# Kernel tuning notes

Hardware: AMD Instinct MI355X
Metric: run time of the kernel (lower is better)

Reference implementation:

```python
import jax, jax.numpy as jnp
import numpy as np

DIM = 32      # state dim (enc_shape[0])
LDIM = 256    # latent dim (enc_shape[-1])
N_AUX = LDIM // 2
AUX_H = 128   # aux hidden
ENC_H = 256   # encoder hidden
T = 64        # n_shifts
N = 1024      # batch
DT = 0.01


def setup_inputs() -> dict:
    key = jax.random.key(0)
    ks = jax.random.split(key, 13)
    def w(k, shape, fan):
        return jax.random.normal(k, shape, jnp.float32) / np.sqrt(fan).astype(np.float32)
    return {
        "xs": jax.random.normal(ks[0], (N, T, DIM), jnp.float32),
        # encoder MLP: dim -> 256 -> 256 -> ldim (last layer has no bias)
        "enc_W1": w(ks[1], (DIM, ENC_H), DIM), "enc_b1": w(ks[2], (ENC_H,), ENC_H),
        "enc_W2": w(ks[3], (ENC_H, ENC_H), ENC_H), "enc_b2": w(ks[4], (ENC_H,), ENC_H),
        "enc_W3": w(ks[5], (ENC_H, LDIM), ENC_H),
        # n_aux independent aux MLPs: dim -> 128 -> 128 -> 2 (last no bias), stacked
        "aux_W1": w(ks[6], (N_AUX, DIM, AUX_H), DIM), "aux_b1": w(ks[7], (N_AUX, AUX_H), AUX_H),
        "aux_W2": w(ks[8], (N_AUX, AUX_H, AUX_H), AUX_H), "aux_b2": w(ks[9], (N_AUX, AUX_H), AUX_H),
        "aux_W3": w(ks[10], (N_AUX, AUX_H, 2), AUX_H),
        # C: Linear(ldim, dim, bias=False); stored as [ldim, dim] so x_next = y @ C_W
        "C_W": w(ks[11], (LDIM, DIM), LDIM),
    }


def reference(xs, enc_W1, enc_b1, enc_W2, enc_b2, enc_W3,
              aux_W1, aux_b1, aux_W2, aux_b2, aux_W3, C_W):
    x0 = xs[:, 0, :]                                    # [N, dim]
    # all n_aux tiny MLPs batched via einsum (instead of python loop)
    h = jax.nn.relu(jnp.einsum('nd,kdh->nkh', x0, aux_W1) + aux_b1)
    h = jax.nn.relu(jnp.einsum('nkh,khg->nkg', h, aux_W2) + aux_b2)
    aux = jnp.einsum('nkh,kho->nko', h, aux_W3)          # [N, n_aux, 2] -> (mu, omega)
    scale = jnp.exp(aux[..., 0] * DT)
    cos = jnp.cos(aux[..., 1] * DT) * scale              # [N, n_aux]
    sin = jnp.sin(aux[..., 1] * DT) * scale

    # encoder over all n_shifts timesteps
    e = jax.nn.relu(xs @ enc_W1 + enc_b1)
    e = jax.nn.relu(e @ enc_W2 + enc_b2)
    e = e @ enc_W3                                       # [N, T, ldim]
    y = jnp.concatenate([xs, e], axis=-1)                # [N, T, dim+ldim]

    # Koopman recurrence. The original builds a block-diagonal [ldim, ldim]
    # matrix of 2x2 rotation-scaling blocks (block k acts on latent pair
    # (2k, 2k+1)) and applies it as a row-vector bmm: out = y_row @ K with
    # K_block = [[cos, sin], [-sin, cos]]. We apply the blocks directly.
    y0 = e[:, 0, :].reshape(N, N_AUX, 2)
    def step(carry, _):
        y1, y2 = carry[..., 0], carry[..., 1]
        yn = jnp.stack([y1 * cos - y2 * sin, y1 * sin + y2 * cos], axis=-1)
        return yn, yn
    _, ys = jax.lax.scan(step, y0, None, length=T - 1)   # [T-1, N, n_aux, 2]
    ys = jnp.moveaxis(ys, 0, 1).reshape(N, T - 1, LDIM)  # [N, T-1, ldim]

    y_lat = jnp.concatenate([e[:, :1, :], ys], axis=1)          # [N, T, ldim]
    x_pred = jnp.concatenate([xs[:, :1, :], ys @ C_W], axis=1)  # [N, T, dim]
    y_pred = jnp.concatenate([x_pred, y_lat], axis=-1)          # [N, T, dim+ldim]
    return y, y_pred
```

## Files before the change

kernel.cpp:

```cpp
#include <hip/hip_runtime.h>
#include <math.h>

#define N_SEQ 1024
#define T_SEQ 64
#define DIMX  32
#define LDIM  256
#define NAUX  128
#define AUXH  128
#define ENCH  256
#define OUTC  288
#define DT    0.01f

typedef short bf16x8 __attribute__((ext_vector_type(8)));
typedef float f32x4  __attribute__((ext_vector_type(4)));
typedef unsigned short ush;

__device__ __forceinline__ ush f2bf(float f) {
    unsigned u = __builtin_bit_cast(unsigned, f);
    unsigned r = u + 0x7fffu + ((u >> 16) & 1u);
    return (ush)(r >> 16);
}
__device__ __forceinline__ float bf2f(ush h) {
    unsigned u = ((unsigned)h) << 16;
    return __builtin_bit_cast(float, u);
}
__device__ __forceinline__ f32x4 mfma16(bf16x8 a, bf16x8 b, f32x4 c) {
    return __builtin_amdgcn_mfma_f32_16x16x32_bf16(a, b, c, 0, 0, 0);
}

#define CV_ENC   139264
#define PREP_CONV_BLOCKS 576
#define PREP_TR_BLOCKS   2560
#define PREP_ENC0_BLOCKS 256
__global__ __launch_bounds__(256) void prep_kernel(
    const float* __restrict__ eW1, const float* __restrict__ eb1,
    const float* __restrict__ eW2, const float* __restrict__ eb2,
    const float* __restrict__ eW3, const float* __restrict__ C_W,
    const float* __restrict__ aW1, const float* __restrict__ aW2,
    const float* __restrict__ xs,
    ush* __restrict__ encw, float* __restrict__ cwt,
    ush* __restrict__ a1h, ush* __restrict__ a1l,
    ush* __restrict__ a2h, ush* __restrict__ a2l,
    float* __restrict__ y)
{
    __shared__ float psm[1152];
    const int b   = blockIdx.x;
    const int tid = threadIdx.x;

    if (b < PREP_CONV_BLOCKS) {
        const int idx = b * 256 + tid;
        if (idx < 8192) {
            int c = idx >> 5, k = idx & 31;
            encw[idx] = f2bf(eW1[k * ENCH + c]);
        } else if (idx < 8192 + 65536) {
            int t = idx - 8192; int c = t >> 8, k = t & 255;
            encw[idx] = f2bf(eW2[k * ENCH + c]);
        } else if (idx < CV_ENC) {
            int t = idx - (8192 + 65536); int c = t >> 8, k = t & 255;
            encw[idx] = f2bf(eW3[k * LDIM + c]);
        } else if (idx < CV_ENC + 8192) {
            int t = idx - CV_ENC; int d = t >> 8, l = t & 255;
            cwt[t] = C_W[l * DIMX + d];
        }
        return;
    }

    if (b < PREP_CONV_BLOCKS + PREP_TR_BLOCKS) {
        float (*tile)[33] = (float(*)[33])psm;
        const int bb0 = b - PREP_CONV_BLOCKS;
        const float* src; ush *dh, *dl; int R, j0, r0;
        if (bb0 < 512) {
            int k = bb0 >> 2; j0 = (bb0 & 3) * 32; r0 = 0; R = 32;
            src = aW1 + (size_t)k * 4096;
            dh = a1h + (size_t)k * 4096; dl = a1l + (size_t)k * 4096;
        } else {
            int bb = bb0 - 512;
            int k = bb >> 4; j0 = ((bb >> 2) & 3) * 32; r0 = (bb & 3) * 32; R = 128;
            src = aW2 + (size_t)k * 16384;
            dh = a2h + (size_t)k * 16384; dl = a2l + (size_t)k * 16384;
        }
        for (int i = tid; i < 1024; i += 256) {
            int rr = i >> 5, jj = i & 31;
            tile[rr][jj] = src[(r0 + rr) * 128 + j0 + jj];
        }
        __syncthreads();
        for (int i = tid; i < 1024; i += 256) {
            int jj = i >> 5, rr = i & 31;
            float w = tile[rr][jj];
            ush hi = f2bf(w);
            int off = (j0 + jj) * R + r0 + rr;
            dh[off] = hi;
            dl[off] = f2bf(w - bf2f(hi));
        }
        return;
    }

    {
        float* Xs  = psm;
        float* Hsf = psm + 128;
        const int c  = tid;
        const int n0 = (b - PREP_CONV_BLOCKS - PREP_TR_BLOCKS) * 4;

        if (tid < 32) {
            int r = tid >> 3, q = tid & 7;
            *(float4*)&Xs[r * 32 + q * 4] =
                *(const float4*)&xs[(size_t)(n0 + r) * (T_SEQ * DIMX) + q * 4];
        }
        __syncthreads();

        float acc[4];
        {
            float w[32];
            #pragma unroll
            for (int d = 0; d < 32; ++d) w[d] = eW1[d * ENCH + c];
            const float bb = eb1[c];
            #pragma unroll
            for (int r = 0; r < 4; ++r) {
                float a = bb;
                #pragma unroll
                for (int d4 = 0; d4 < 8; ++d4) {
                    float4 xv = *(const float4*)&Xs[r * 32 + d4 * 4];
                    a += xv.x * w[d4*4] + xv.y * w[d4*4+1] + xv.z * w[d4*4+2] + xv.w * w[d4*4+3];
                }
                acc[r] = a;
            }
            #pragma unroll
            for (int r = 0; r < 4; ++r) Hsf[r * 256 + c] = fmaxf(acc[r], 0.f);
        }
        __syncthreads();
        {
            const float bb = eb2[c];
            #pragma unroll
            for (int r = 0; r < 4; ++r) acc[r] = bb;
            for (int hc = 0; hc < 8; ++hc) {
                float w[32];
                #pragma unroll
                for (int i = 0; i < 32; ++i) w[i] = eW2[(hc * 32 + i) * ENCH + c];
                #pragma unroll
                for (int r = 0; r < 4; ++r) {
                    float a = acc[r];
                    #pragma unroll
                    for (int h4 = 0; h4 < 8; ++h4) {
                        float4 hv = *(const float4*)&Hsf[r * 256 + hc * 32 + h4 * 4];
                        a += hv.x * w[h4*4] + hv.y * w[h4*4+1] + hv.z * w[h4*4+2] + hv.w * w[h4*4+3];
                    }
                    acc[r] = a;
                }
            }
            __syncthreads();
            #pragma unroll
            for (int r = 0; r < 4; ++r) Hsf[r * 256 + c] = fmaxf(acc[r], 0.f);
        }
        __syncthreads();
        {
            #pragma unroll
            for (int r = 0; r < 4; ++r) acc[r] = 0.f;
            for (int hc = 0; hc < 8; ++hc) {
                float w[32];
                #pragma unroll
                for (int i = 0; i < 32; ++i) w[i] = eW3[(hc * 32 + i) * LDIM + c];
                #pragma unroll
                for (int r = 0; r < 4; ++r) {
                    float a = acc[r];
                    #pragma unroll
                    for (int h4 = 0; h4 < 8; ++h4) {
                        float4 hv = *(const float4*)&Hsf[r * 256 + hc * 32 + h4 * 4];
                        a += hv.x * w[h4*4] + hv.y * w[h4*4+1] + hv.z * w[h4*4+2] + hv.w * w[h4*4+3];
                    }
                    acc[r] = a;
                }
            }
        }
        #pragma unroll
        for (int r = 0; r < 4; ++r)
            y[((size_t)(n0 + r) * T_SEQ) * OUTC + DIMX + c] = acc[r];
    }
}

__global__ __launch_bounds__(256) void main_kernel(
    const float* __restrict__ xs,
    const ush* __restrict__ W1h, const ush* __restrict__ W1l,
    const float* __restrict__ ab1,
    const ush* __restrict__ W2h, const ush* __restrict__ W2l,
    const float* __restrict__ ab2,
    const float* __restrict__ aW3,
    float* __restrict__ a_ws, float* __restrict__ th_ws,
    const ush* __restrict__ W1T, const float* __restrict__ eb1,
    const ush* __restrict__ W2T, const float* __restrict__ eb2,
    const ush* __restrict__ W3T,
    float* __restrict__ y)
{
    __shared__ __align__(16) char smem[46080];
    const int tid = threadIdx.x;
    const int wv  = tid >> 6;
    const int ln  = tid & 63;
    const int lr  = ln & 15;
    const int g   = ln >> 4;

    if (blockIdx.x < 2048) {
        ush (*x0h)[40]  = (ush(*)[40]) (smem);
        ush (*x0l)[40]  = (ush(*)[40]) (smem + 5120);
        ush (*h1h)[136] = (ush(*)[136])(smem + 10240);
        ush (*h1l)[136] = (ush(*)[136])(smem + 27648);
        float* p3       = (float*)     (smem + 45056);

        const int k   = blockIdx.x >> 4;
        const int n0  = (blockIdx.x & 15) << 6;
        const int cb  = wv * 32;

        for (int i = tid; i < 512; i += 256) {
            int r = i >> 3, qd = i & 7;
            float4 v = *(const float4*)&xs[(size_t)(n0 + r) * (T_SEQ * DIMX) + qd * 4];
            short4 hs, ls;
            float vv[4] = {v.x, v.y, v.z, v.w};
            short* hp = (short*)&hs; short* lp = (short*)&ls;
            #pragma unroll
            for (int u = 0; u < 4; ++u) {
                ush hi = f2bf(vv[u]);
                hp[u] = (short)hi;
                lp[u] = (short)f2bf(vv[u] - bf2f(hi));
            }
            *(short4*)&x0h[r][qd * 4] = hs;
            *(short4*)&x0l[r][qd * 4] = ls;
        }
        __syncthreads();

        {
            const ush* W1hk = W1h + (size_t)k * 4096;
            const ush* W1lk = W1l + (size_t)k * 4096;
            bf16x8 bh[2], bl[2];
            #pragma unroll
            for (int ct = 0; ct < 2; ++ct) {
                int off = (cb + ct * 16 + lr) * 32 + g * 8;
                bh[ct] = *(const bf16x8*)&W1hk[off];
                bl[ct] = *(const bf16x8*)&W1lk[off];
            }
            f32x4 acc[4][2];
            #pragma unroll
            for (int rt = 0; rt < 4; ++rt) {
                bf16x8 ah = *(const bf16x8*)&x0h[rt * 16 + lr][g * 8];
                bf16x8 al = *(const bf16x8*)&x0l[rt * 16 + lr][g * 8];
                #pragma unroll
                for (int ct = 0; ct < 2; ++ct) {
                    f32x4 z = {0.f, 0.f, 0.f, 0.f};
                    z = mfma16(ah, bl[ct], z);
                    z = mfma16(al, bh[ct], z);
                    acc[rt][ct] = mfma16(ah, bh[ct], z);
                }
            }
            #pragma unroll
            for (int ct = 0; ct < 2; ++ct) {
                const int col = cb + ct * 16 + lr;
                const float bb = ab1[k * 128 + col];
                #pragma unroll
                for (int rt = 0; rt < 4; ++rt)
                    #pragma unroll
                    for (int i = 0; i < 4; ++i) {
                        float h = fmaxf(acc[rt][ct][i] + bb, 0.f);
                        ush hi = f2bf(h);
                        int row = rt * 16 + g * 4 + i;
                        h1h[row][col] = hi;
                        h1l[row][col] = f2bf(h - bf2f(hi));
                    }
            }
        }
        __syncthreads();

        {
            const ush* W2hk = W2h + (size_t)k * 16384;
            const ush* W2lk = W2l + (size_t)k * 16384;
            f32x4 acc[4][2];
            #pragma unroll
            for (int rt = 0; rt < 4; ++rt)
                #pragma unroll
                for (int ct = 0; ct < 2; ++ct) acc[rt][ct] = (f32x4){0.f,0.f,0.f,0.f};

            #pragma unroll
            for (int kk = 0; kk < 4; ++kk) {
                bf16x8 bh[2], bl[2], ah[4], al[4];
                #pragma unroll
                for (int ct = 0; ct < 2; ++ct) {
                    int off = (cb + ct * 16 + lr) * 128 + kk * 32 + g * 8;
                    bh[ct] = *(const bf16x8*)&W2hk[off];
                    bl[ct] = *(const bf16x8*)&W2lk[off];
                }
                #pragma unroll
                for (int rt = 0; rt < 4; ++rt) {
                    ah[rt] = *(const bf16x8*)&h1h[rt * 16 + lr][kk * 32 + g * 8];
                    al[rt] = *(const bf16x8*)&h1l[rt * 16 + lr][kk * 32 + g * 8];
                }
                #pragma unroll
                for (int rt = 0; rt < 4; ++rt)
                    #pragma unroll
                    for (int ct = 0; ct < 2; ++ct) {
                        f32x4 z = acc[rt][ct];
                        z = mfma16(ah[rt], bl[ct], z);
                        z = mfma16(al[rt], bh[ct], z);
                        acc[rt][ct] = mfma16(ah[rt], bh[ct], z);
                    }
            }
            __syncthreads();
            #pragma unroll
            for (int ct = 0; ct < 2; ++ct) {
                const int col = cb + ct * 16 + lr;
                const float bb = ab2[k * 128 + col];
                #pragma unroll
                for (int rt = 0; rt < 4; ++rt)
                    #pragma unroll
                    for (int i = 0; i < 4; ++i) {
                        float h = fmaxf(acc[rt][ct][i] + bb, 0.f);
                        ush hi = f2bf(h);
                        int row = rt * 16 + g * 4 + i;
                        h1h[row][col] = hi;
                        h1l[row][col] = f2bf(h - bf2f(hi));
                    }
            }
        }
        __syncthreads();

        {
            const int hh = tid >> 7, r = tid & 127, n = r >> 1, o = r & 1;
            const float* W3k = aW3 + (size_t)k * (AUXH * 2);
            float s = 0.f;
            #pragma unroll
            for (int h8 = hh * 64; h8 < hh * 64 + 64; h8 += 8) {
                bf16x8 vh = *(const bf16x8*)&h1h[n][h8];
                bf16x8 vl = *(const bf16x8*)&h1l[n][h8];
                #pragma unroll
                for (int u = 0; u < 8; ++u) {
                    float hv = bf2f((ush)vh[u]) + bf2f((ush)vl[u]);
                    s += hv * W3k[(h8 + u) * 2 + o];
                }
            }
            p3[tid] = s;
        }
        __syncthreads();
        if (tid < 128) {
            const int n = tid >> 1, o = tid & 1;
            float v = (p3[tid] + p3[tid + 128]) * DT;
            float* dst = o ? th_ws : a_ws;
            dst[(size_t)(n0 + n) * NAUX + k] = v;
        }
        return;
    }

    {
        float* Xf = (float*)smem;
        ush*   Hs = (ush*)(smem + 9216);

        const int cb  = wv * 64;
        const size_t row0 = (size_t)(blockIdx.x - 2048) * 64;

        {
            const float4* src = (const float4*)(xs + row0 * DIMX);
            for (int i = tid; i < 512; i += 256) {
                int r = i >> 3, q = i & 7;
                *(float4*)&Xf[r * 36 + q * 4] = src[i];
            }
        }
        __syncthreads();

        {
            f32x4 acc[4][4];
            bf16x8 bfr[4], afr[4];
            #pragma unroll
            for (int ct = 0; ct < 4; ++ct)
                bfr[ct] = *(const bf16x8*)&W1T[(cb + ct * 16 + lr) * 32 + g * 8];
            #pragma unroll
            for (int rt = 0; rt < 4; ++rt) {
                const float* xp = &Xf[(rt * 16 + lr) * 36 + g * 8];
                float4 u = *(const float4*)xp;
                float4 v = *(const float4*)(xp + 4);
                bf16x8 t;
                t[0]=(short)f2bf(u.x); t[1]=(short)f2bf(u.y); t[2]=(short)f2bf(u.z); t[3]=(short)f2bf(u.w);
                t[4]=(short)f2bf(v.x); t[5]=(short)f2bf(v.y); t[6]=(short)f2bf(v.z); t[7]=(short)f2bf(v.w);
                afr[rt] = t;
            }
            #pragma unroll
            for (int rt = 0; rt < 4; ++rt)
                #pragma unroll
                for (int ct = 0; ct < 4; ++ct) {
                    f32x4 z = {0.f, 0.f, 0.f, 0.f};
                    acc[rt][ct] = mfma16(afr[rt], bfr[ct], z);
                }
            #pragma unroll
            for (int ct = 0; ct < 4; ++ct) {
                const float bb = eb1[cb + ct * 16 + lr];
                #pragma unroll
                for (int rt = 0; rt < 4; ++rt)
                    #pragma unroll
                    for (int i = 0; i < 4; ++i) {
                        float h = fmaxf(acc[rt][ct][i] + bb, 0.f);
                        Hs[(rt * 16 + g * 4 + i) * 264 + cb + ct * 16 + lr] = f2bf(h);
                    }
            }
        }
        __syncthreads();

        int wrow[4], hoff[4];
        #pragma unroll
        for (int ct = 0; ct < 4; ++ct) wrow[ct] = (cb + ct * 16 + lr) * 256 + g * 8;
        #pragma unroll
        for (int rt = 0; rt < 4; ++rt) hoff[rt] = (rt * 16 + lr) * 264 + g * 8;

        {
            f32x4 acc[4][4];
            #pragma unroll
            for (int rt = 0; rt < 4; ++rt)
                #pragma unroll
                for (int ct = 0; ct < 4; ++ct) acc[rt][ct] = (f32x4){0.f,0.f,0.f,0.f};
            #pragma unroll 2
            for (int kk = 0; kk < 8; ++kk) {
                bf16x8 bfr[4], afr[4];
                #pragma unroll
                for (int ct = 0; ct < 4; ++ct)
                    bfr[ct] = *(const bf16x8*)&W2T[wrow[ct] + kk * 32];
                #pragma unroll
                for (int rt = 0; rt < 4; ++rt)
                    afr[rt] = *(const bf16x8*)&Hs[hoff[rt] + kk * 32];
                #pragma unroll
                for (int rt = 0; rt < 4; ++rt)
                    #pragma unroll
                    for (int ct = 0; ct < 4; ++ct)
                        acc[rt][ct] = mfma16(afr[rt], bfr[ct], acc[rt][ct]);
            }
            __syncthreads();
            #pragma unroll
            for (int ct = 0; ct < 4; ++ct) {
                const float bb = eb2[cb + ct * 16 + lr];
                #pragma unroll
                for (int rt = 0; rt < 4; ++rt)
                    #pragma unroll
                    for (int i = 0; i < 4; ++i) {
                        float h = fmaxf(acc[rt][ct][i] + bb, 0.f);
                        Hs[(rt * 16 + g * 4 + i) * 264 + cb + ct * 16 + lr] = f2bf(h);
                    }
            }
        }
        __syncthreads();

        {
            f32x4 acc[4][4];
            #pragma unroll
            for (int rt = 0; rt < 4; ++rt)
                #pragma unroll
                for (int ct = 0; ct < 4; ++ct) acc[rt][ct] = (f32x4){0.f,0.f,0.f,0.f};
            #pragma unroll 2
            for (int kk = 0; kk < 8; ++kk) {
                bf16x8 bfr[4], afr[4];
                #pragma unroll
                for (int ct = 0; ct < 4; ++ct)
                    bfr[ct] = *(const bf16x8*)&W3T[wrow[ct] + kk * 32];
                #pragma unroll
                for (int rt = 0; rt < 4; ++rt)
                    afr[rt] = *(const bf16x8*)&Hs[hoff[rt] + kk * 32];
                #pragma unroll
                for (int rt = 0; rt < 4; ++rt)
                    #pragma unroll
                    for (int ct = 0; ct < 4; ++ct)
                        acc[rt][ct] = mfma16(afr[rt], bfr[ct], acc[rt][ct]);
            }
            __syncthreads();

            float* HsF = (float*)Hs;
            const int r  = tid >> 3;
            const int ce = tid & 7;

            #pragma unroll
            for (int p = 0; p < 2; ++p) {
                #pragma unroll
                for (int rt = 2 * p; rt < 2 * p + 2; ++rt)
                    #pragma unroll
                    for (int ct = 0; ct < 4; ++ct)
                        #pragma unroll
                        for (int i = 0; i < 4; ++i)
                            HsF[((rt - 2 * p) * 16 + g * 4 + i) * 264 + cb + ct * 16 + lr]
                                = acc[rt][ct][i];
                __syncthreads();
                const int rloc = p * 32 + r;
                float* dstrow = &y[(row0 + rloc) * OUTC];
                #pragma unroll
                for (int j = 0; j < 9; ++j) {
                    int f4 = j * 8 + ce;
                    float4 v;
                    if (f4 < 8) v = *(const float4*)&Xf[rloc * 36 + f4 * 4];
                    else        v = *(const float4*)&HsF[r * 264 + (f4 - 8) * 4];
                    if (!(rloc == 0 && f4 >= 8))
                        *(float4*)&dstrow[f4 * 4] = v;
                }
                __syncthreads();
            }
        }
    }
}

__global__ __launch_bounds__(256) void scan3_kernel(
    const float* __restrict__ xs,
    const float* __restrict__ a_ws, const float* __restrict__ th_ws,
    const float* __restrict__ cwt,
    const float* __restrict__ y,
    float* __restrict__ yp)
{
    __shared__ float ys_lds[16][256];

    const int n = blockIdx.x >> 2;
    const int q = blockIdx.x & 3;
    const int e = threadIdx.x;
    const int k = e >> 1;

    const float* yrow0 = y + (size_t)n * T_SEQ * OUTC + DIMX;
    float2 y0 = *(const float2*)&yrow0[e & ~1];
    const float a  = a_ws [n * NAUX + k];
    const float th = th_ws[n * NAUX + k];

    const float m = expf(a);
    float ss, cc; sincosf(th, &ss, &cc);
    const float zr = m * cc, zi = m * ss;

    float pr = zr, pi = zi;
    #pragma unroll
    for (int s2 = 0; s2 < 4; ++s2) {
        float nr = pr * pr - pi * pi;
        pi = 2.f * pr * pi; pr = nr;
    }
    float wr = 1.f, wi = 0.f;
    for (int j = 0; j < q; ++j) {
        float nr = wr * pr - wi * pi;
        wi = wr * pi + wi * pr; wr = nr;
    }

    const bool imag = e & 1;
    float* ypn = yp + (size_t)n * T_SEQ * OUTC;

    #pragma unroll 4
    for (int tl = 0; tl < 16; ++tl) {
        const int t = q * 16 + tl;
        float val = imag ? (y0.x * wi + y0.y * wr)
                         : (y0.x * wr - y0.y * wi);
        ypn[(size_t)t * OUTC + DIMX + e] = val;
        ys_lds[tl][(e + ((tl >> 1) & 7) * 4) & 255] = val;
        float nwr = wr * zr - wi * zi;
        wi = wr * zi + wi * zr;
        wr = nwr;
    }
    __syncthreads();

    const int d   = e >> 3;
    const int tg  = e & 7;
    const int tl0 = tg * 2, tl1 = tl0 + 1;
    const float* cwd = cwt + d * 256;
    const int rot = tg * 4;

    float s0 = 0.f, s1 = 0.f;
    #pragma unroll 8
    for (int l = 0; l < 256; l += 4) {
        const int c0 = (l + rot) & 255;
        float4 wv = *(const float4*)&cwd[l];
        float4 ya = *(const float4*)&ys_lds[tl0][c0];
        float4 yb = *(const float4*)&ys_lds[tl1][c0];
        s0 += ya.x * wv.x + ya.y * wv.y + ya.z * wv.z + ya.w * wv.w;
        s1 += yb.x * wv.x + yb.y * wv.y + yb.z * wv.z + yb.w * wv.w;
    }
    const int t0 = q * 16 + tl0;
    const int t1 = q * 16 + tl1;
    float o0 = (t0 == 0) ? xs[(size_t)n * T_SEQ * DIMX + d] : s0;
    ypn[(size_t)t0 * OUTC + d] = o0;
    ypn[(size_t)t1 * OUTC + d] = s1;
}

extern "C" void kernel_launch(void* const* d_in, const int* in_sizes, int n_in,
                              void* d_out, int out_size, void* d_ws, size_t ws_size,
                              hipStream_t stream)
{
    const float* xs   = (const float*)d_in[0];
    const float* eW1  = (const float*)d_in[1];
    const float* eb1  = (const float*)d_in[2];
    const float* eW2  = (const float*)d_in[3];
    const float* eb2  = (const float*)d_in[4];
    const float* eW3  = (const float*)d_in[5];
    const float* aW1  = (const float*)d_in[6];
    const float* ab1  = (const float*)d_in[7];
    const float* aW2  = (const float*)d_in[8];
    const float* ab2  = (const float*)d_in[9];
    const float* aW3  = (const float*)d_in[10];
    const float* C_W  = (const float*)d_in[11];

    float* y  = (float*)d_out;
    float* yp = y + (size_t)N_SEQ * T_SEQ * OUTC;

    float* a_ws  = (float*)d_ws;
    float* th_ws = a_ws + (size_t)N_SEQ * NAUX;
    ush* encw = (ush*)(th_ws + (size_t)N_SEQ * NAUX);
    ush* W1T = encw;
    ush* W2T = encw + 8192;
    ush* W3T = encw + 8192 + 65536;
    ush* a1h = encw + CV_ENC;
    ush* a1l = a1h + 524288;
    ush* a2h = a1l + 524288;
    ush* a2l = a2h + 2097152;
    float* cwt = (float*)(a2l + 2097152);

    prep_kernel<<<PREP_CONV_BLOCKS + PREP_TR_BLOCKS + PREP_ENC0_BLOCKS, 256, 0, stream>>>(
        eW1, eb1, eW2, eb2, eW3, C_W, aW1, aW2, xs,
        encw, cwt, a1h, a1l, a2h, a2l, y);
    main_kernel<<<3072, 256, 0, stream>>>(
        xs, a1h, a1l, ab1, a2h, a2l, ab2, aW3, a_ws, th_ws,
        W1T, eb1, W2T, eb2, W3T, y);
    scan3_kernel<<<N_SEQ * 4, 256, 0, stream>>>(xs, a_ws, th_ws, cwt, y, yp);
}
```

Measured before the change: 166.3 us.

## Split fused aux/encoder kernel into two kernels with smaller aux tiles

The combined main kernel, which branched on block index between the aux-MLP and encoder paths, is split into separate auxm and encm kernels. Each now gets its own LDS footprint, so the encoder path is no longer limited by the larger union allocation and the aux path uses far less LDS. The aux kernel halves its row tile (32 rows, 4096 blocks), stages W3 in shared memory, and reduces the final layer over four partial sums instead of two. The cost is an extra kernel launch and serialization between the two stages instead of their blocks co-scheduling in one grid, plus twice as many aux weight fetches because there are twice as many row tiles.

```diff
diff --git a/kernel.cpp b/kernel.cpp
--- a/kernel.cpp
+++ b/kernel.cpp
@@ -177,319 +177,323 @@
     }
 }
 
-__global__ __launch_bounds__(256) void main_kernel(
+__global__ __launch_bounds__(256) void auxm_kernel(
     const float* __restrict__ xs,
     const ush* __restrict__ W1h, const ush* __restrict__ W1l,
-    const float* __restrict__ ab1,
+    const float* __restrict__ b1,
     const ush* __restrict__ W2h, const ush* __restrict__ W2l,
-    const float* __restrict__ ab2,
-    const float* __restrict__ aW3,
-    float* __restrict__ a_ws, float* __restrict__ th_ws,
-    const ush* __restrict__ W1T, const float* __restrict__ eb1,
-    const ush* __restrict__ W2T, const float* __restrict__ eb2,
-    const ush* __restrict__ W3T,
-    float* __restrict__ y)
+    const float* __restrict__ b2,
+    const float* __restrict__ W3,
+    float* __restrict__ a_ws, float* __restrict__ th_ws)
 {
-    __shared__ __align__(16) char smem[46080];
+    const int k   = blockIdx.x >> 5;
+    const int n0  = (blockIdx.x & 31) << 5;
     const int tid = threadIdx.x;
     const int wv  = tid >> 6;
     const int ln  = tid & 63;
     const int lr  = ln & 15;
     const int g   = ln >> 4;
-
-    if (blockIdx.x < 2048) {
-        ush (*x0h)[40]  = (ush(*)[40]) (smem);
-        ush (*x0l)[40]  = (ush(*)[40]) (smem + 5120);
-        ush (*h1h)[136] = (ush(*)[136])(smem + 10240);
-        ush (*h1l)[136] = (ush(*)[136])(smem + 27648);
-        float* p3       = (float*)     (smem + 45056);
-
-        const int k   = blockIdx.x >> 4;
-        const int n0  = (blockIdx.x & 15) << 6;
-        const int cb  = wv * 32;
-
+    const int cb  = wv * 32;
+
+    __shared__ ush   x0h[32][40];
+    __shared__ ush   x0l[32][40];
+    __shared__ ush   h1h[32][136];
+    __shared__ ush   h1l[32][136];
+    __shared__ float w3s[256];
+    __shared__ float p3[256];
+
+    for (int i = tid; i < 256; i += 256) {
+        int r = i >> 3, qd = i & 7;
+        float4 v = *(const float4*)&xs[(size_t)(n0 + r) * (T_SEQ * DIMX) + qd * 4];
+        short4 hs, ls;
+        float vv[4] = {v.x, v.y, v.z, v.w};
+        short* hp = (short*)&hs; short* lp = (short*)&ls;
+        #pragma unroll
+        for (int u = 0; u < 4; ++u) {
+            ush hi = f2bf(vv[u]);
+            hp[u] = (short)hi;
+            lp[u] = (short)f2bf(vv[u] - bf2f(hi));
+        }
+        *(short4*)&x0h[r][qd * 4] = hs;
+        *(short4*)&x0l[r][qd * 4] = ls;
+    }
+    w3s[tid] = W3[(size_t)k * (AUXH * 2) + tid];
+    __syncthreads();
+
+    {
+        const ush* W1hk = W1h + (size_t)k * 4096;
+        const ush* W1lk = W1l + (size_t)k * 4096;
+        bf16x8 bh[2], bl[2];
+        #pragma unroll
+        for (int ct = 0; ct < 2; ++ct) {
+            int off = (cb + ct * 16 + lr) * 32 + g * 8;
+            bh[ct] = *(const bf16x8*)&W1hk[off];
+            bl[ct] = *(const bf16x8*)&W1lk[off];
+        }
+        f32x4 acc[2][2];
+        #pragma unroll
+        for (int rt = 0; rt < 2; ++rt) {
+            bf16x8 ah = *(const bf16x8*)&x0h[rt * 16 + lr][g * 8];
+            bf16x8 al = *(const bf16x8*)&x0l[rt * 16 + lr][g * 8];
+            #pragma unroll
+            for (int ct = 0; ct < 2; ++ct) {
+                f32x4 z = {0.f, 0.f, 0.f, 0.f};
+                z = mfma16(ah, bl[ct], z);
+                z = mfma16(al, bh[ct], z);
+                acc[rt][ct] = mfma16(ah, bh[ct], z);
+            }
+        }
+        #pragma unroll
+        for (int ct = 0; ct < 2; ++ct) {
+            const int col = cb + ct * 16 + lr;
+            const float bb = b1[k * 128 + col];
+            #pragma unroll
+            for (int rt = 0; rt < 2; ++rt)
+                #pragma unroll
+                for (int i = 0; i < 4; ++i) {
+                    float h = fmaxf(acc[rt][ct][i] + bb, 0.f);
+                    ush hi = f2bf(h);
+                    int row = rt * 16 + g * 4 + i;
+                    h1h[row][col] = hi;
+                    h1l[row][col] = f2bf(h - bf2f(hi));
+                }
+        }
+    }
+    __syncthreads();
+
+    {
+        const ush* W2hk = W2h + (size_t)k * 16384;
+        const ush* W2lk = W2l + (size_t)k * 16384;
+        f32x4 acc[2][2];
+        #pragma unroll
+        for (int rt = 0; rt < 2; ++rt)
+            #pragma unroll
+            for (int ct = 0; ct < 2; ++ct) acc[rt][ct] = (f32x4){0.f,0.f,0.f,0.f};
+
+        #pragma unroll
+        for (int kk = 0; kk < 4; ++kk) {
+            bf16x8 bh[2], bl[2], ah[2], al[2];
+            #pragma unroll
+            for (int ct = 0; ct < 2; ++ct) {
+                int off = (cb + ct * 16 + lr) * 128 + kk * 32 + g * 8;
+                bh[ct] = *(const bf16x8*)&W2hk[off];
+                bl[ct] = *(const bf16x8*)&W2lk[off];
+            }
+            #pragma unroll
+            for (int rt = 0; rt < 2; ++rt) {
+                ah[rt] = *(const bf16x8*)&h1h[rt * 16 + lr][kk * 32 + g * 8];
+                al[rt] = *(const bf16x8*)&h1l[rt * 16 + lr][kk * 32 + g * 8];
+            }
+            #pragma unroll
+            for (int rt = 0; rt < 2; ++rt)
+                #pragma unroll
+                for (int ct = 0; ct < 2; ++ct) {
+                    f32x4 z = acc[rt][ct];
+                    z = mfma16(ah[rt], bl[ct], z);
+                    z = mfma16(al[rt], bh[ct], z);
+                    acc[rt][ct] = mfma16(ah[rt], bh[ct], z);
+                }
+        }
+        __syncthreads();
+        #pragma unroll
+        for (int ct = 0; ct < 2; ++ct) {
+            const int col = cb + ct * 16 + lr;
+            const float bb = b2[k * 128 + col];
+            #pragma unroll
+            for (int rt = 0; rt < 2; ++rt)
+                #pragma unroll
+                for (int i = 0; i < 4; ++i) {
+                    float h = fmaxf(acc[rt][ct][i] + bb, 0.f);
+                    ush hi = f2bf(h);
+                    int row = rt * 16 + g * 4 + i;
+                    h1h[row][col] = hi;
+                    h1l[row][col] = f2bf(h - bf2f(hi));
+                }
+        }
+    }
+    __syncthreads();
+
+    {
+        const int n = tid >> 3, o = (tid >> 2) & 1, q = tid & 3;
+        float s = 0.f;
+        #pragma unroll
+        for (int h8 = q * 32; h8 < q * 32 + 32; h8 += 8) {
+            bf16x8 vh = *(const bf16x8*)&h1h[n][h8];
+            bf16x8 vl = *(const bf16x8*)&h1l[n][h8];
+            #pragma unroll
+            for (int u = 0; u < 8; ++u) {
+                float hv = bf2f((ush)vh[u]) + bf2f((ush)vl[u]);
+                s += hv * w3s[(h8 + u) * 2 + o];
+            }
+        }
+        p3[tid] = s;
+    }
+    __syncthreads();
+    if (tid < 64) {
+        const int n = tid >> 1, o = tid & 1;
+        const int base = n * 8 + o * 4;
+        float v = (p3[base] + p3[base + 1] + p3[base + 2] + p3[base + 3]) * DT;
+        float* dst = o ? th_ws : a_ws;
+        dst[(size_t)(n0 + n) * NAUX + k] = v;
+    }
+}
+
+__global__ __launch_bounds__(256) void encm_kernel(
+    const float* __restrict__ xs,
+    const ush* __restrict__ W1T, const float* __restrict__ b1,
+    const ush* __restrict__ W2T, const float* __restrict__ b2,
+    const ush* __restrict__ W3T,
+    float* __restrict__ y)
+{
+    __shared__ float Xf[64 * 36];
+    __shared__ ush   Hs[64 * 264];
+
+    const int tid = threadIdx.x;
+    const int wv  = tid >> 6;
+    const int ln  = tid & 63;
+    const int lr  = ln & 15;
+    const int g   = ln >> 4;
+    const int cb  = wv * 64;
+    const size_t row0 = (size_t)blockIdx.x * 64;
+
+    {
+        const float4* src = (const float4*)(xs + row0 * DIMX);
         for (int i = tid; i < 512; i += 256) {
-            int r = i >> 3, qd = i & 7;
-            float4 v = *(const float4*)&xs[(size_t)(n0 + r) * (T_SEQ * DIMX) + qd * 4];
-            short4 hs, ls;
-            float vv[4] = {v.x, v.y, v.z, v.w};
-            short* hp = (short*)&hs; short* lp = (short*)&ls;
-            #pragma unroll
-            for (int u = 0; u < 4; ++u) {
-                ush hi = f2bf(vv[u]);
-                hp[u] = (short)hi;
-                lp[u] = (short)f2bf(vv[u] - bf2f(hi));
-            }
-            *(short4*)&x0h[r][qd * 4] = hs;
-            *(short4*)&x0l[r][qd * 4] = ls;
+            int r = i >> 3, q = i & 7;
+            *(float4*)&Xf[r * 36 + q * 4] = src[i];
+        }
+    }
+    __syncthreads();
+
+    {
+        f32x4 acc[4][4];
+        bf16x8 bfr[4], afr[4];
+        #pragma unroll
+        for (int ct = 0; ct < 4; ++ct)
+            bfr[ct] = *(const bf16x8*)&W1T[(cb + ct * 16 + lr) * 32 + g * 8];
+        #pragma unroll
+        for (int rt = 0; rt < 4; ++rt) {
+            const float* xp = &Xf[(rt * 16 + lr) * 36 + g * 8];
+            float4 u = *(const float4*)xp;
+            float4 v = *(const float4*)(xp + 4);
+            bf16x8 t;
+            t[0]=(short)f2bf(u.x); t[1]=(short)f2bf(u.y); t[2]=(short)f2bf(u.z); t[3]=(short)f2bf(u.w);
+            t[4]=(short)f2bf(v.x); t[5]=(short)f2bf(v.y); t[6]=(short)f2bf(v.z); t[7]=(short)f2bf(v.w);
+            afr[rt] = t;
+        }
+        #pragma unroll
+        for (int rt = 0; rt < 4; ++rt)
+            #pragma unroll
+            for (int ct = 0; ct < 4; ++ct) {
+                f32x4 z = {0.f, 0.f, 0.f, 0.f};
+                acc[rt][ct] = mfma16(afr[rt], bfr[ct], z);
+            }
+        #pragma unroll
+        for (int ct = 0; ct < 4; ++ct) {
+            const float bb = b1[cb + ct * 16 + lr];
+            #pragma unroll
+            for (int rt = 0; rt < 4; ++rt)
+                #pragma unroll
+                for (int i = 0; i < 4; ++i) {
+                    float h = fmaxf(acc[rt][ct][i] + bb, 0.f);
+                    Hs[(rt * 16 + g * 4 + i) * 264 + cb + ct * 16 + lr] = f2bf(h);
+                }
+        }
+    }
+    __syncthreads();
+
+    int wrow[4], hoff[4];
+    #pragma unroll
+    for (int ct = 0; ct < 4; ++ct) wrow[ct] = (cb + ct * 16 + lr) * 256 + g * 8;
+    #pragma unroll
+    for (int rt = 0; rt < 4; ++rt) hoff[rt] = (rt * 16 + lr) * 264 + g * 8;
+
+    {
+        f32x4 acc[4][4];
+        #pragma unroll
+        for (int rt = 0; rt < 4; ++rt)
+            #pragma unroll
+            for (int ct = 0; ct < 4; ++ct) acc[rt][ct] = (f32x4){0.f,0.f,0.f,0.f};
+        #pragma unroll 2
+        for (int kk = 0; kk < 8; ++kk) {
+            bf16x8 bfr[4], afr[4];
+            #pragma unroll
+            for (int ct = 0; ct < 4; ++ct)
+                bfr[ct] = *(const bf16x8*)&W2T[wrow[ct] + kk * 32];
+            #pragma unroll
+            for (int rt = 0; rt < 4; ++rt)
+                afr[rt] = *(const bf16x8*)&Hs[hoff[rt] + kk * 32];
+            #pragma unroll
+            for (int rt = 0; rt < 4; ++rt)
+                #pragma unroll
+                for (int ct = 0; ct < 4; ++ct)
+                    acc[rt][ct] = mfma16(afr[rt], bfr[ct], acc[rt][ct]);
         }
         __syncthreads();
-
-        {
-            const ush* W1hk = W1h + (size_t)k * 4096;
-            const ush* W1lk = W1l + (size_t)k * 4096;
-            bf16x8 bh[2], bl[2];
-            #pragma unroll
-            for (int ct = 0; ct < 2; ++ct) {
-                int off = (cb + ct * 16 + lr) * 32 + g * 8;
-                bh[ct] = *(const bf16x8*)&W1hk[off];
-                bl[ct] = *(const bf16x8*)&W1lk[off];
-            }
-            f32x4 acc[4][2];
-            #pragma unroll
-            for (int rt = 0; rt < 4; ++rt) {
-                bf16x8 ah = *(const bf16x8*)&x0h[rt * 16 + lr][g * 8];
-                bf16x8 al = *(const bf16x8*)&x0l[rt * 16 + lr][g * 8];
-                #pragma unroll
-                for (int ct = 0; ct < 2; ++ct) {
-                    f32x4 z = {0.f, 0.f, 0.f, 0.f};
-                    z = mfma16(ah, bl[ct], z);
-                    z = mfma16(al, bh[ct], z);
-                    acc[rt][ct] = mfma16(ah, bh[ct], z);
-                }
-            }
-            #pragma unroll
-            for (int ct = 0; ct < 2; ++ct) {
-                const int col = cb + ct * 16 + lr;
-                const float bb = ab1[k * 128 + col];
-                #pragma unroll
-                for (int rt = 0; rt < 4; ++rt)
+        #pragma unroll
+        for (int ct = 0; ct < 4; ++ct) {
+            const float bb = b2[cb + ct * 16 + lr];
+            #pragma unroll
+            for (int rt = 0; rt < 4; ++rt)
+                #pragma unroll
+                for (int i = 0; i < 4; ++i) {
+                    float h = fmaxf(acc[rt][ct][i] + bb, 0.f);
+                    Hs[(rt * 16 + g * 4 + i) * 264 + cb + ct * 16 + lr] = f2bf(h);
+                }
+        }
+    }
+    __syncthreads();
+
+    {
+        f32x4 acc[4][4];
+        #pragma unroll
+        for (int rt = 0; rt < 4; ++rt)
+            #pragma unroll
+            for (int ct = 0; ct < 4; ++ct) acc[rt][ct] = (f32x4){0.f,0.f,0.f,0.f};
+        #pragma unroll 2
+        for (int kk = 0; kk < 8; ++kk) {
+            bf16x8 bfr[4], afr[4];
+            #pragma unroll
+            for (int ct = 0; ct < 4; ++ct)
+                bfr[ct] = *(const bf16x8*)&W3T[wrow[ct] + kk * 32];
+            #pragma unroll
+            for (int rt = 0; rt < 4; ++rt)
+                afr[rt] = *(const bf16x8*)&Hs[hoff[rt] + kk * 32];
+            #pragma unroll
+            for (int rt = 0; rt < 4; ++rt)
+                #pragma unroll
+                for (int ct = 0; ct < 4; ++ct)
+                    acc[rt][ct] = mfma16(afr[rt], bfr[ct], acc[rt][ct]);
+        }
+        __syncthreads();
+
+        float* HsF = (float*)Hs;
+        const int r  = tid >> 3;
+        const int ce = tid & 7;
+
+        #pragma unroll
+        for (int p = 0; p < 2; ++p) {
+            #pragma unroll
+            for (int rt = 2 * p; rt < 2 * p + 2; ++rt)
+                #pragma unroll
+                for (int ct = 0; ct < 4; ++ct)
                     #pragma unroll
-                    for (int i = 0; i < 4; ++i) {
-                        float h = fmaxf(acc[rt][ct][i] + bb, 0.f);
-                        ush hi = f2bf(h);
-                        int row = rt * 16 + g * 4 + i;
-                        h1h[row][col] = hi;
-                        h1l[row][col] = f2bf(h - bf2f(hi));
-                    }
-            }
-        }
-        __syncthreads();
-
-        {
-            const ush* W2hk = W2h + (size_t)k * 16384;
-            const ush* W2lk = W2l + (size_t)k * 16384;
-            f32x4 acc[4][2];
-            #pragma unroll
-            for (int rt = 0; rt < 4; ++rt)
-                #pragma unroll
-                for (int ct = 0; ct < 2; ++ct) acc[rt][ct] = (f32x4){0.f,0.f,0.f,0.f};
-
-            #pragma unroll
-            for (int kk = 0; kk < 4; ++kk) {
-                bf16x8 bh[2], bl[2], ah[4], al[4];
-                #pragma unroll
-                for (int ct = 0; ct < 2; ++ct) {
-                    int off = (cb + ct * 16 + lr) * 128 + kk * 32 + g * 8;
-                    bh[ct] = *(const bf16x8*)&W2hk[off];
-                    bl[ct] = *(const bf16x8*)&W2lk[off];
-                }
-                #pragma unroll
-                for (int rt = 0; rt < 4; ++rt) {
-                    ah[rt] = *(const bf16x8*)&h1h[rt * 16 + lr][kk * 32 + g * 8];
-                    al[rt] = *(const bf16x8*)&h1l[rt * 16 + lr][kk * 32 + g * 8];
-                }
-                #pragma unroll
-                for (int rt = 0; rt < 4; ++rt)
-                    #pragma unroll
-                    for (int ct = 0; ct < 2; ++ct) {
-                        f32x4 z = acc[rt][ct];
-                        z = mfma16(ah[rt], bl[ct], z);
-                        z = mfma16(al[rt], bh[ct], z);
-                        acc[rt][ct] = mfma16(ah[rt], bh[ct], z);
-                    }
-            }
+                    for (int i = 0; i < 4; ++i)
+                        HsF[((rt - 2 * p) * 16 + g * 4 + i) * 264 + cb + ct * 16 + lr]
+                            = acc[rt][ct][i];
             __syncthreads();
-            #pragma unroll
-            for (int ct = 0; ct < 2; ++ct) {
-                const int col = cb + ct * 16 + lr;
-                const float bb = ab2[k * 128 + col];
-                #pragma unroll
-                for (int rt = 0; rt < 4; ++rt)
-                    #pragma unroll
-                    for (int i = 0; i < 4; ++i) {
-                        float h = fmaxf(acc[rt][ct][i] + bb, 0.f);
-                        ush hi = f2bf(h);
-                        int row = rt * 16 + g * 4 + i;
-                        h1h[row][col] = hi;
-                        h1l[row][col] = f2bf(h - bf2f(hi));
-                    }
-            }
-        }
-        __syncthreads();
-
-        {
-            const int hh = tid >> 7, r = tid & 127, n = r >> 1, o = r & 1;
-            const float* W3k = aW3 + (size_t)k * (AUXH * 2);
-            float s = 0.f;
-            #pragma unroll
-            for (int h8 = hh * 64; h8 < hh * 64 + 64; h8 += 8) {
-                bf16x8 vh = *(const bf16x8*)&h1h[n][h8];
-                bf16x8 vl = *(const bf16x8*)&h1l[n][h8];
-                #pragma unroll
-                for (int u = 0; u < 8; ++u) {
-                    float hv = bf2f((ush)vh[u]) + bf2f((ush)vl[u]);
-                    s += hv * W3k[(h8 + u) * 2 + o];
-                }
-            }
-            p3[tid] = s;
-        }
-        __syncthreads();
-        if (tid < 128) {
-            const int n = tid >> 1, o = tid & 1;
-            float v = (p3[tid] + p3[tid + 128]) * DT;
-            float* dst = o ? th_ws : a_ws;
-            dst[(size_t)(n0 + n) * NAUX + k] = v;
-        }
-        return;
-    }
-
-    {
-        float* Xf = (float*)smem;
-        ush*   Hs = (ush*)(smem + 9216);
-
-        const int cb  = wv * 64;
-        const size_t row0 = (size_t)(blockIdx.x - 2048) * 64;
-
-        {
-            const float4* src = (const float4*)(xs + row0 * DIMX);
-            for (int i = tid; i < 512; i += 256) {
-                int r = i >> 3, q = i & 7;
-                *(float4*)&Xf[r * 36 + q * 4] = src[i];
-            }
-        }
-        __syncthreads();
-
-        {
-            f32x4 acc[4][4];
-            bf16x8 bfr[4], afr[4];
-            #pragma unroll
-            for (int ct = 0; ct < 4; ++ct)
-                bfr[ct] = *(const bf16x8*)&W1T[(cb + ct * 16 + lr) * 32 + g * 8];
-            #pragma unroll
-            for (int rt = 0; rt < 4; ++rt) {
-                const float* xp = &Xf[(rt * 16 + lr) * 36 + g * 8];
-                float4 u = *(const float4*)xp;
-                float4 v = *(const float4*)(xp + 4);
-                bf16x8 t;
-                t[0]=(short)f2bf(u.x); t[1]=(short)f2bf(u.y); t[2]=(short)f2bf(u.z); t[3]=(short)f2bf(u.w);
-                t[4]=(short)f2bf(v.x); t[5]=(short)f2bf(v.y); t[6]=(short)f2bf(v.z); t[7]=(short)f2bf(v.w);
-                afr[rt] = t;
-            }
-            #pragma unroll
-            for (int rt = 0; rt < 4; ++rt)
-                #pragma unroll
-                for (int ct = 0; ct < 4; ++ct) {
-                    f32x4 z = {0.f, 0.f, 0.f, 0.f};
-                    acc[rt][ct] = mfma16(afr[rt], bfr[ct], z);
-                }
-            #pragma unroll
-            for (int ct = 0; ct < 4; ++ct) {
-                const float bb = eb1[cb + ct * 16 + lr];
-                #pragma unroll
-                for (int rt = 0; rt < 4; ++rt)
-                    #pragma unroll
-                    for (int i = 0; i < 4; ++i) {
-                        float h = fmaxf(acc[rt][ct][i] + bb, 0.f);
-                        Hs[(rt * 16 + g * 4 + i) * 264 + cb + ct * 16 + lr] = f2bf(h);
-                    }
-            }
-        }
-        __syncthreads();
-
-        int wrow[4], hoff[4];
-        #pragma unroll
-        for (int ct = 0; ct < 4; ++ct) wrow[ct] = (cb + ct * 16 + lr) * 256 + g * 8;
-        #pragma unroll
-        for (int rt = 0; rt < 4; ++rt) hoff[rt] = (rt * 16 + lr) * 264 + g * 8;
-
-        {
-            f32x4 acc[4][4];
-            #pragma unroll
-            for (int rt = 0; rt < 4; ++rt)
-                #pragma unroll
-                for (int ct = 0; ct < 4; ++ct) acc[rt][ct] = (f32x4){0.f,0.f,0.f,0.f};
-            #pragma unroll 2
-            for (int kk = 0; kk < 8; ++kk) {
-                bf16x8 bfr[4], afr[4];
-                #pragma unroll
-                for (int ct = 0; ct < 4; ++ct)
-                    bfr[ct] = *(const bf16x8*)&W2T[wrow[ct] + kk * 32];
-                #pragma unroll
-                for (int rt = 0; rt < 4; ++rt)
-                    afr[rt] = *(const bf16x8*)&Hs[hoff[rt] + kk * 32];
-                #pragma unroll
-                for (int rt = 0; rt < 4; ++rt)
-                    #pragma unroll
-                    for (int ct = 0; ct < 4; ++ct)
-                        acc[rt][ct] = mfma16(afr[rt], bfr[ct], acc[rt][ct]);
+            const int rloc = p * 32 + r;
+            float* dstrow = &y[(row0 + rloc) * OUTC];
+            #pragma unroll
+            for (int j = 0; j < 9; ++j) {
+                int f4 = j * 8 + ce;
+                float4 v;
+                if (f4 < 8) v = *(const float4*)&Xf[rloc * 36 + f4 * 4];
+                else        v = *(const float4*)&HsF[r * 264 + (f4 - 8) * 4];
+                if (!(rloc == 0 && f4 >= 8))
+                    *(float4*)&dstrow[f4 * 4] = v;
             }
             __syncthreads();
-            #pragma unroll
-            for (int ct = 0; ct < 4; ++ct) {
-                const float bb = eb2[cb + ct * 16 + lr];
-                #pragma unroll
-                for (int rt = 0; rt < 4; ++rt)
-                    #pragma unroll
-                    for (int i = 0; i < 4; ++i) {
-                        float h = fmaxf(acc[rt][ct][i] + bb, 0.f);
-                        Hs[(rt * 16 + g * 4 + i) * 264 + cb + ct * 16 + lr] = f2bf(h);
-                    }
-            }
-        }
-        __syncthreads();
-
-        {
-            f32x4 acc[4][4];
-            #pragma unroll
-            for (int rt = 0; rt < 4; ++rt)
-                #pragma unroll
-                for (int ct = 0; ct < 4; ++ct) acc[rt][ct] = (f32x4){0.f,0.f,0.f,0.f};
-            #pragma unroll 2
-            for (int kk = 0; kk < 8; ++kk) {
-                bf16x8 bfr[4], afr[4];
-                #pragma unroll
-                for (int ct = 0; ct < 4; ++ct)
-                    bfr[ct] = *(const bf16x8*)&W3T[wrow[ct] + kk * 32];
-                #pragma unroll
-                for (int rt = 0; rt < 4; ++rt)
-                    afr[rt] = *(const bf16x8*)&Hs[hoff[rt] + kk * 32];
-                #pragma unroll
-                for (int rt = 0; rt < 4; ++rt)
-                    #pragma unroll
-                    for (int ct = 0; ct < 4; ++ct)
-                        acc[rt][ct] = mfma16(afr[rt], bfr[ct], acc[rt][ct]);
-            }
-            __syncthreads();
-
-            float* HsF = (float*)Hs;
-            const int r  = tid >> 3;
-            const int ce = tid & 7;
-
-            #pragma unroll
-            for (int p = 0; p < 2; ++p) {
-                #pragma unroll
-                for (int rt = 2 * p; rt < 2 * p + 2; ++rt)
-                    #pragma unroll
-                    for (int ct = 0; ct < 4; ++ct)
-                        #pragma unroll
-                        for (int i = 0; i < 4; ++i)
-                            HsF[((rt - 2 * p) * 16 + g * 4 + i) * 264 + cb + ct * 16 + lr]
-                                = acc[rt][ct][i];
-                __syncthreads();
-                const int rloc = p * 32 + r;
-                float* dstrow = &y[(row0 + rloc) * OUTC];
-                #pragma unroll
-                for (int j = 0; j < 9; ++j) {
-                    int f4 = j * 8 + ce;
-                    float4 v;
-                    if (f4 < 8) v = *(const float4*)&Xf[rloc * 36 + f4 * 4];
-                    else        v = *(const float4*)&HsF[r * 264 + (f4 - 8) * 4];
-                    if (!(rloc == 0 && f4 >= 8))
-                        *(float4*)&dstrow[f4 * 4] = v;
-                }
-                __syncthreads();
-            }
         }
     }
 }
@@ -603,8 +607,9 @@
     prep_kernel<<<PREP_CONV_BLOCKS + PREP_TR_BLOCKS + PREP_ENC0_BLOCKS, 256, 0, stream>>>(
         eW1, eb1, eW2, eb2, eW3, C_W, aW1, aW2, xs,
         encw, cwt, a1h, a1l, a2h, a2l, y);
-    main_kernel<<<3072, 256, 0, stream>>>(
-        xs, a1h, a1l, ab1, a2h, a2l, ab2, aW3, a_ws, th_ws,
-        W1T, eb1, W2T, eb2, W3T, y);
+    auxm_kernel<<<128 * 32, 256, 0, stream>>>(
+        xs, a1h, a1l, ab1, a2h, a2l, ab2, aW3, a_ws, th_ws);
+    encm_kernel<<<N_SEQ * T_SEQ / 64, 256, 0, stream>>>(
+        xs, W1T, eb1, W2T, eb2, W3T, y);
     scan3_kernel<<<N_SEQ * 4, 256, 0, stream>>>(xs, a_ws, th_ws, cwt, y, yp);
 }
```

New measurement: 172.3 us. +3.6%, slower.
